# Kernel optimization log

Measured on AMD Instinct MI355X. Metric: run time of the kernel, lower is better.

## Reference

```python
import jax, jax.numpy as jnp
import numpy as np

MAX_SET_SIZE = 32  # f1_query_max_set_size


def setup_inputs() -> dict:
    key = jax.random.key(0)
    k1, k2, k3, k4 = jax.random.split(key, 4)
    B, Lq, L, d_qk, d_v = 8, 512, 4096, 64, 64
    q = jax.random.normal(k1, (B, Lq, d_qk), dtype=jnp.float32)
    k = jax.random.normal(k2, (B, L, d_qk), dtype=jnp.float32)
    v = jax.random.normal(k3, (B, L, d_v), dtype=jnp.float32)
    mask = jax.random.randint(k4, (B * Lq, L), 0, 2).astype(bool)
    return {"q": q, "k": k, "v": v, "mask": mask}


def _query_conditioned_subset_pool(rank_scores, v, batch_idx, mask, max_set_size):
    # rank_scores/mask: [N, L]; v: [B, L, d_v]
    N, L = rank_scores.shape
    keep = min(max_set_size, L)
    neg_inf = jnp.finfo(rank_scores.dtype).min
    masked_scores = jnp.where(mask, rank_scores.astype(jnp.float32), neg_inf)
    _, top_idx = jax.lax.top_k(masked_scores, keep)          # [N, keep]
    picked = jnp.take_along_axis(mask, top_idx, axis=1)
    sortable = jnp.where(picked, top_idx, L)                 # sentinel L for unpicked
    sortable = jnp.sort(sortable, axis=1)                    # restore index order
    picked = sortable < L
    safe_idx = jnp.where(picked, sortable, 0)                # [N, keep]
    sel_v = v[batch_idx[:, None], safe_idx]                  # [N, keep, d_v]
    sel_scores = jnp.take_along_axis(rank_scores, safe_idx, axis=1)
    sel_scores = jnp.where(picked, sel_scores, neg_inf)
    attn = jax.nn.softmax(sel_scores, axis=1)
    non_empty = picked.any(axis=1, keepdims=True)
    attn = jnp.where(picked & non_empty, attn, jnp.zeros_like(attn))
    return jnp.einsum('nk,nkd->nd', attn.astype(sel_v.dtype), sel_v)


def reference(q, k, v, mask):
    B, Lq, d_qk = q.shape
    L = k.shape[1]
    d_v = v.shape[-1]
    scale = 1.0 / float(np.sqrt(d_qk))
    # rank_scores [B, Lq, L] -> flat chains [B*Lq, L]
    rank_scores = jnp.einsum('bqd,bld->bql', q, k) * scale
    rs_flat = rank_scores.reshape(B * Lq, L)
    batch_idx = jnp.repeat(jnp.arange(B), Lq)
    # f1 = mean over masked support: sum_v / clamp(count, 1)
    mask_f = mask.astype(q.dtype)                            # [B*Lq, L]
    count = jnp.clip(mask_f.sum(axis=1), 1.0, None)          # [B*Lq]
    sum_v = jnp.einsum('bql,bld->bqd', mask_f.reshape(B, Lq, L), v).reshape(B * Lq, d_v)
    mean_out = sum_v / count[:, None]
    # f1_query_mode='add': query-conditioned restricted pooling over top-k subset
    q_ctx = _query_conditioned_subset_pool(rs_flat, v, batch_idx, mask, MAX_SET_SIZE)
    out = mean_out + q_ctx
    return out.reshape(B, Lq, d_v)
```

## Files before the change

### kernel.cpp

```cpp
#include <hip/hip_runtime.h>
#include <float.h>
#include <math.h>

#define LQ   512
#define LL   4096
#define DD   64
#define KEEP 32
#define NB   8
#define NROWS (NB * LQ)

#define WS_VT    (NROWS * LL)
#define WS_PC    (WS_VT + (NB * DD * LL) / 2)
#define WS_TOTAL (WS_PC + 4 * NROWS)

#define MASKED_KEY 0x00800000u

typedef short  bf16x8 __attribute__((ext_vector_type(8)));
typedef float  f32x4  __attribute__((ext_vector_type(4)));

__device__ __forceinline__ float dot4(float4 a, float4 b) {
    return a.x * b.x + a.y * b.y + a.z * b.z + a.w * b.w;
}
__device__ __forceinline__ unsigned short f2bf(float f) {
    unsigned int u = __float_as_uint(f);
    return (unsigned short)((u + 0x7FFFu + ((u >> 16) & 1u)) >> 16);
}

#define TP_LB 256
__global__ __launch_bounds__(256) void k_vt(
    const float* __restrict__ v, unsigned short* __restrict__ vt)
{
    __shared__ unsigned short tile[DD][TP_LB + 8];
    const int t  = threadIdx.x;
    const int b  = blockIdx.x >> 4;
    const int l0 = (blockIdx.x & 15) * TP_LB;

    const float4* vg = reinterpret_cast<const float4*>(v + ((size_t)b * LL + l0) * DD);
    #pragma unroll
    for (int i = 0; i < 16; ++i) {
        int j = t + 256 * i;
        float4 f = vg[j];
        int l = j >> 4, dq = (j & 15) * 4;
        tile[dq + 0][l] = f2bf(f.x);
        tile[dq + 1][l] = f2bf(f.y);
        tile[dq + 2][l] = f2bf(f.z);
        tile[dq + 3][l] = f2bf(f.w);
    }
    __syncthreads();
    const int d = t >> 2, seg = t & 3;
    const uint4* src = reinterpret_cast<const uint4*>(&tile[d][seg * 64]);
    uint4* dst = reinterpret_cast<uint4*>(vt + ((size_t)b * DD + d) * LL + l0 + seg * 64);
    #pragma unroll
    for (int i = 0; i < 8; ++i) dst[i] = src[i];
}

__global__ __launch_bounds__(256) void k_mean(
    const int* __restrict__ mask,
    const unsigned short* __restrict__ vt,
    float* __restrict__ out,
    float* __restrict__ pcnt)
{
    __shared__ float sums[4][4][16][16];
    __shared__ float cnt_s[4][16];

    const int t     = threadIdx.x;
    const int wave  = t >> 6;
    const int lane  = t & 63;
    const int lcq   = blockIdx.x & 3;
    const int rg    = blockIdx.x >> 2;
    const int n0    = rg * 16;
    const int b     = n0 / LQ;
    const int row_a = lane & 15;
    const int chunk = lane >> 4;
    const int lb    = lcq * 1024 + wave * 256;

    const int* mrow = mask + (size_t)(n0 + row_a) * LL + lb + chunk * 8;
    const unsigned short* vbase = vt + (size_t)b * DD * LL + lb + chunk * 8;

    f32x4 acc[4];
    #pragma unroll
    for (int dt = 0; dt < 4; ++dt) acc[dt] = (f32x4){0.f, 0.f, 0.f, 0.f};
    int cnt = 0;

    for (int l0 = 0; l0 < 256; l0 += 32) {
        int4 ma = *reinterpret_cast<const int4*>(mrow + l0);
        int4 mb = *reinterpret_cast<const int4*>(mrow + l0 + 4);
        cnt += (ma.x != 0) + (ma.y != 0) + (ma.z != 0) + (ma.w != 0)
             + (mb.x != 0) + (mb.y != 0) + (mb.z != 0) + (mb.w != 0);
        unsigned int p[4];
        p[0] = (ma.x ? 0x3F80u : 0u) | (ma.y ? 0x3F800000u : 0u);
        p[1] = (ma.z ? 0x3F80u : 0u) | (ma.w ? 0x3F800000u : 0u);
        p[2] = (mb.x ? 0x3F80u : 0u) | (mb.y ? 0x3F800000u : 0u);
        p[3] = (mb.z ? 0x3F80u : 0u) | (mb.w ? 0x3F800000u : 0u);
        bf16x8 afrag = *reinterpret_cast<bf16x8*>(p);
        #pragma unroll
        for (int dt = 0; dt < 4; ++dt) {
            bf16x8 bfrag = *reinterpret_cast<const bf16x8*>(
                vbase + (size_t)(dt * 16 + row_a) * LL + l0);
            acc[dt] = __builtin_amdgcn_mfma_f32_16x16x32_bf16(afrag, bfrag, acc[dt], 0, 0, 0);
        }
    }
    cnt += __shfl_xor(cnt, 16);
    cnt += __shfl_xor(cnt, 32);
    if (lane < 16) cnt_s[wave][lane] = (float)cnt;
    #pragma unroll
    for (int dt = 0; dt < 4; ++dt)
        #pragma unroll
        for (int r = 0; r < 4; ++r)
            sums[wave][dt][chunk * 4 + r][row_a] = acc[dt][r];
    __syncthreads();

    const int d = t & 63, rgrp = t >> 6;
    #pragma unroll
    for (int rr = 0; rr < 4; ++rr) {
        const int row = rgrp * 4 + rr;
        float s = sums[0][d >> 4][row][d & 15] + sums[1][d >> 4][row][d & 15]
                + sums[2][d >> 4][row][d & 15] + sums[3][d >> 4][row][d & 15];
        float c = cnt_s[0][row] + cnt_s[1][row] + cnt_s[2][row] + cnt_s[3][row];
        atomicAdd(&out[(size_t)(n0 + row) * DD + d], s);
        if (d == 0) pcnt[lcq * NROWS + n0 + row] = c;
    }
}

__global__ __launch_bounds__(256) void k_scores(
    const float* __restrict__ q,
    const float* __restrict__ kmat,
    const int*   __restrict__ mask,
    float*       __restrict__ ws_sc)
{
    const int t    = threadIdx.x;
    const int wave = t >> 6;
    const int lane = t & 63;
    const int lc   = blockIdx.x & 15;
    const int rg   = blockIdx.x >> 4;
    const int n0   = rg * 16;
    const int b    = n0 / LQ;
    const int l    = lc * 256 + wave * 64 + lane;

    const float4* kr = reinterpret_cast<const float4*>(kmat + ((size_t)b * LL + l) * DD);
    float4 kreg[16];
    #pragma unroll
    for (int i = 0; i < 16; ++i) kreg[i] = kr[i];

    int mreg[16];
    #pragma unroll
    for (int p = 0; p < 16; ++p)
        mreg[p] = mask[(size_t)(n0 + p) * LL + l];

    const int qb = __builtin_amdgcn_readfirstlane(n0 * DD);
    #pragma unroll
    for (int p = 0; p < 16; ++p) {
        const float4* qp = reinterpret_cast<const float4*>(q + qb + p * DD);
        float ax = 0.f, ay = 0.f, az = 0.f, aw = 0.f;
        #pragma unroll
        for (int i = 0; i < 16; ++i) {
            float4 qv = qp[i];
            ax = fmaf(qv.x, kreg[i].x, ax);
            ay = fmaf(qv.y, kreg[i].y, ay);
            az = fmaf(qv.z, kreg[i].z, az);
            aw = fmaf(qv.w, kreg[i].w, aw);
        }
        float acc = ax + ay + az + aw;
        ws_sc[(size_t)(n0 + p) * LL + l] = mreg[p] ? acc * 0.125f : -FLT_MAX;
    }
}

__global__ __launch_bounds__(256, 3) void k_select(
    const float* __restrict__ vmat,
    const float* __restrict__ ws,
    const float* __restrict__ pcnt,
    float*       __restrict__ out)
{
    __shared__ unsigned int hist[4][256];
    __shared__ unsigned int selKey[4][KEEP];
    __shared__ int          selIdx[4][KEEP];
    __shared__ float        wsel[4][KEEP];
    __shared__ int          selCnt[4], eqCnt[4];

    const int t    = threadIdx.x;
    const int wave = t >> 6;
    const int lane = t & 63;
    const int row  = blockIdx.x * 4 + wave;
    const int b    = row / LQ;

    float o = out[(size_t)row * DD + lane];
    {
        float cc = pcnt[row] + pcnt[NROWS + row]
                 + pcnt[2 * NROWS + row] + pcnt[3 * NROWS + row];
        if (cc < 1.f) cc = 1.f;
        o /= cc;
    }

    unsigned int key[64];
    {
        const float4* sg = reinterpret_cast<const float4*>(ws) + (size_t)row * (LL / 4);
        #pragma unroll
        for (int i = 0; i < 16; ++i) {
            float4 f = sg[lane + 64 * i];
            float vals[4] = { f.x, f.y, f.z, f.w };
            #pragma unroll
            for (int c = 0; c < 4; ++c) {
                unsigned int u = __float_as_uint(vals[c]);
                key[4 * i + c] = ((int)u < 0) ? ~u : (u | 0x80000000u);
            }
        }
    }

    unsigned int prefix = 0, quota = KEEP;
    #pragma unroll
    for (int pass = 0; pass < 4; ++pass) {
        const int shift = 24 - 8 * pass;
        const unsigned int hs = (pass == 0) ? 0u : (unsigned int)(32 - 8 * pass);
        reinterpret_cast<uint4*>(hist[wave])[lane] = make_uint4(0u, 0u, 0u, 0u);
        __asm__ volatile("s_waitcnt lgkmcnt(0)" ::: "memory");
        #pragma unroll
        for (int e = 0; e < 64; ++e) {
            bool act = (pass == 0) || ((key[e] >> hs) == prefix);
            if (act) atomicAdd(&hist[wave][(key[e] >> shift) & 255u], 1u);
        }
        __asm__ volatile("s_waitcnt lgkmcnt(0)" ::: "memory");
        uint4 h = reinterpret_cast<const uint4*>(hist[wave])[lane];
        unsigned int s4  = h.x + h.y + h.z + h.w;
        unsigned int suf = s4;
        #pragma unroll
        for (int off = 1; off < 64; off <<= 1) {
            unsigned int v = (unsigned int)__shfl_down((int)suf, off);
            if (lane + off < 64) suf += v;
        }
        unsigned int above = suf - s4;
        bool cond = (suf >= quota) && (above < quota);
        unsigned int Bq = 0, nq = 0;
        if (cond) {
            unsigned int hb[4] = { h.x, h.y, h.z, h.w };
            unsigned int run = above;
            int Bj = 0;
            #pragma unroll
            for (int j = 3; j >= 0; --j) {
                unsigned int nb = run + hb[j];
                if (nb >= quota) { Bj = j; break; }
                run = nb;
            }
            Bq = (unsigned int)(lane * 4 + Bj);
            nq = quota - run;
        }
        unsigned long long bal = __ballot(cond);
        int src = __ffsll(bal) - 1;
        Bq = (unsigned int)__shfl((int)Bq, src);
        nq = (unsigned int)__shfl((int)nq, src);
        prefix = (prefix << 8) | Bq;
        quota  = nq;
    }
    const unsigned int T = prefix;
    const bool take_eq = (T != MASKED_KEY);

    if (lane < KEEP) { wsel[wave][lane] = 0.f; selIdx[wave][lane] = 0; }
    if (lane == 0)   { selCnt[wave] = 0; eqCnt[wave] = 0; }
    __asm__ volatile("s_waitcnt lgkmcnt(0)" ::: "memory");
    #pragma unroll
    for (int e = 0; e < 64; ++e) {
        unsigned int k = key[e];
        if (k > T) {
            int slot = atomicAdd(&selCnt[wave], 1);
            selKey[wave][slot] = k;
            selIdx[wave][slot] = 256 * (e >> 2) + 4 * lane + (e & 3);
        } else if (take_eq && k == T) {
            int t2 = atomicAdd(&eqCnt[wave], 1);
            if (t2 < (int)quota) {
                int slot = atomicAdd(&selCnt[wave], 1);
                selKey[wave][slot] = k;
                selIdx[wave][slot] = 256 * (e >> 2) + 4 * lane + (e & 3);
            }
        }
    }
    __asm__ volatile("s_waitcnt lgkmcnt(0)" ::: "memory");
    const int S = selCnt[wave];

    if (S > 0) {
        float vj = -FLT_MAX;
        if (lane < S) {
            unsigned int kk = selKey[wave][lane];
            unsigned int u = (kk & 0x80000000u) ? (kk ^ 0x80000000u) : ~kk;
            vj = __uint_as_float(u);
        }
        float mx = vj;
        #pragma unroll
        for (int off = 1; off < 64; off <<= 1) mx = fmaxf(mx, __shfl_xor(mx, off));
        float e = (lane < S) ? expf(vj - mx) : 0.f;
        float sum = e;
        #pragma unroll
        for (int off = 1; off < 64; off <<= 1) sum += __shfl_xor(sum, off);
        if (lane < S) wsel[wave][lane] = e / sum;
        __asm__ volatile("s_waitcnt lgkmcnt(0)" ::: "memory");
        const float* vb = vmat + (size_t)b * LL * DD + lane;
        #pragma unroll
        for (int j = 0; j < KEEP; ++j) {
            float wj = wsel[wave][j];
            int   ij = selIdx[wave][j];
            o += wj * vb[(size_t)ij * DD];
        }
    }
    out[(size_t)row * DD + lane] = o;
}

#define QT   2
#define NT   256
#define NTILES (LL / NT)

__global__ __launch_bounds__(NT, 4) void ga_fused_fb(
    const float* __restrict__ q, const float* __restrict__ kmat,
    const float* __restrict__ vmat, const int* __restrict__ mask,
    float* __restrict__ out)
{
    __shared__ float sc[QT][LL];
    __shared__ float q_s[QT][DD];
    __shared__ unsigned long long mbits[QT][LL / 64];
    __shared__ float redv[4][QT][DD];
    __shared__ float mean_s[QT][DD];
    __shared__ int   count_s[QT];
    __shared__ int   sel_idx[QT][KEEP];
    __shared__ float sel_val[QT][KEEP];
    __shared__ int   sel_cnt[QT];
    __shared__ float wred[4];
    __shared__ int   ired[4];
    __shared__ int   brk;
    __shared__ float wgt[QT][KEEP];

    const int t = threadIdx.x, wave = t >> 6, lane = t & 63;
    const int n0 = blockIdx.x * QT, b = n0 / LQ;

    if (t < QT) sel_cnt[t] = 0;
    if (t < QT * DD) q_s[t >> 6][t & 63] = q[(size_t)(n0 + (t >> 6)) * DD + (t & 63)];
    __syncthreads();

    const float4* q4_0 = reinterpret_cast<const float4*>(&q_s[0][0]);
    const float4* q4_1 = reinterpret_cast<const float4*>(&q_s[1][0]);
    for (int tile = 0; tile < NTILES; ++tile) {
        int l = tile * NT + t;
        const float4* kr = reinterpret_cast<const float4*>(kmat + (size_t)(b * LL + l) * DD);
        float d0 = 0.f, d1 = 0.f;
        #pragma unroll
        for (int i = 0; i < 16; ++i) {
            float4 kk = kr[i], qa = q4_0[i], qb = q4_1[i];
            d0 += kk.x * qa.x + kk.y * qa.y + kk.z * qa.z + kk.w * qa.w;
            d1 += kk.x * qb.x + kk.y * qb.y + kk.z * qb.z + kk.w * qb.w;
        }
        int mv0 = mask[(size_t)n0 * LL + l];
        int mv1 = mask[(size_t)(n0 + 1) * LL + l];
        unsigned long long b0 = __ballot(mv0 != 0);
        unsigned long long b1 = __ballot(mv1 != 0);
        if (lane == 0) { mbits[0][tile * 4 + wave] = b0; mbits[1][tile * 4 + wave] = b1; }
        sc[0][l] = mv0 ? d0 * 0.125f : -FLT_MAX;
        sc[1][l] = mv1 ? d1 * 0.125f : -FLT_MAX;
    }
    __syncthreads();

    if (wave < QT) {
        int c = (int)__popcll(mbits[wave][lane]);
        for (int off = 32; off >= 1; off >>= 1) c += __shfl_down(c, off);
        if (lane == 0) count_s[wave] = c;
    }
    {
        float acc0 = 0.f, acc1 = 0.f;
        const int g = wave, d = lane;
        for (int wi = 0; wi < LL / 64; ++wi) {
            unsigned long long w0 = mbits[0][wi], w1 = mbits[1][wi];
            const float* vp = vmat + (size_t)(b * LL + wi * 64 + g) * DD + d;
            #pragma unroll 4
            for (int ii = 0; ii < 16; ++ii) {
                int sh = g + 4 * ii;
                float vv = vp[(size_t)(4 * ii) * DD];
                if ((w0 >> sh) & 1ULL) acc0 += vv;
                if ((w1 >> sh) & 1ULL) acc1 += vv;
            }
        }
        redv[g][0][d] = acc0; redv[g][1][d] = acc1;
    }
    __syncthreads();
    if (t < QT * DD) {
        int qt = t >> 6, dd = t & 63;
        float s2 = redv[0][qt][dd] + redv[1][qt][dd] + redv[2][qt][dd] + redv[3][qt][dd];
        int c = count_s[qt]; if (c < 1) c = 1;
        mean_s[qt][dd] = s2 / (float)c;
    }
    __syncthreads();

    for (int qt = 0; qt < QT; ++qt) {
        for (int s = 0; s < KEEP; ++s) {
            float m = -FLT_MAX; int mi = LL;
            for (int j = 0; j < NTILES; ++j) {
                int l = j * NT + t;
                float val = sc[qt][l];
                if (val > m) { m = val; mi = l; }
            }
            for (int off = 32; off >= 1; off >>= 1) {
                float ov = __shfl_down(m, off);
                int   oi = __shfl_down(mi, off);
                if (ov > m || (ov == m && oi < mi)) { m = ov; mi = oi; }
            }
            if (lane == 0) { wred[wave] = m; ired[wave] = mi; }
            __syncthreads();
            if (t == 0) {
                float bv = wred[0]; int bi = ired[0];
                for (int w2 = 1; w2 < 4; ++w2) {
                    float ov = wred[w2]; int oi = ired[w2];
                    if (ov > bv || (ov == bv && oi < bi)) { bv = ov; bi = oi; }
                }
                if (bv > -FLT_MAX) {
                    sel_idx[qt][s] = bi; sel_val[qt][s] = bv; sel_cnt[qt] = s + 1;
                    sc[qt][bi] = -FLT_MAX; brk = 0;
                } else brk = 1;
            }
            __syncthreads();
            if (brk) break;
        }
    }

    if (wave < QT) {
        int qt = wave, S = sel_cnt[qt];
        if (S > 0) {
            float mx = sel_val[qt][0];
            float e = 0.f;
            if (lane < S) e = expf(sel_val[qt][lane] - mx);
            float ssum = e;
            for (int off = 32; off >= 1; off >>= 1) ssum += __shfl_xor(ssum, off);
            if (lane < S) wgt[qt][lane] = e / ssum;
        }
    }
    __syncthreads();
    if (wave < QT) {
        int qt = wave, S = sel_cnt[qt];
        float o = mean_s[qt][lane];
        for (int j = 0; j < S; ++j)
            o += wgt[qt][j] * vmat[(size_t)(b * LL + sel_idx[qt][j]) * DD + lane];
        out[(size_t)(n0 + qt) * DD + lane] = o;
    }
}

extern "C" void kernel_launch(void* const* d_in, const int* in_sizes, int n_in,
                              void* d_out, int out_size, void* d_ws, size_t ws_size,
                              hipStream_t stream) {
    const float* q    = (const float*)d_in[0];
    const float* kmat = (const float*)d_in[1];
    const float* vmat = (const float*)d_in[2];
    const int*   mask = (const int*)d_in[3];
    float* out = (float*)d_out;

    const size_t need = (size_t)WS_TOTAL * sizeof(float);
    if (ws_size >= need) {
        float* ws = (float*)d_ws;
        unsigned short* vt = (unsigned short*)(ws + WS_VT);
        float* pcnt = ws + WS_PC;
        hipMemsetAsync(out, 0, (size_t)NROWS * DD * sizeof(float), stream);
        hipLaunchKernelGGL(k_scores, dim3(4096), dim3(256), 0, stream,
                           q, kmat, mask, ws);
        hipLaunchKernelGGL(k_vt, dim3(NB * 16), dim3(256), 0, stream, vmat, vt);
        hipLaunchKernelGGL(k_mean, dim3((NROWS / 16) * 4), dim3(256), 0, stream,
                           mask, vt, out, pcnt);
        hipLaunchKernelGGL(k_select, dim3(NROWS / 4), dim3(256), 0, stream,
                           vmat, ws, pcnt, out);
    } else {
        hipLaunchKernelGGL(ga_fused_fb, dim3(NROWS / QT), dim3(NT), 0, stream,
                           q, kmat, vmat, mask, out);
    }
}
```

Measured before the change: 253.7 us.

## Fuse masked mean accumulation into score kernel using ballot-packed mask bits

Removes the separate k_mean kernel and computes the masked V sum and count inside k_scores. The mask values it already loads are packed with ballots into shared bitmasks and fed as bf16 MFMA operands against the transposed V. The intent is to avoid reading the 64 MB int mask a second time. The costs are more global atomics (16x more blocks each add partial sums into out and a single pcnt), an extra memset, and higher register and LDS pressure in k_scores.

```diff
diff --git a/kernel.cpp b/kernel.cpp
--- a/kernel.cpp
+++ b/kernel.cpp
@@ -54,80 +54,19 @@
     for (int i = 0; i < 8; ++i) dst[i] = src[i];
 }
 
-__global__ __launch_bounds__(256) void k_mean(
-    const int* __restrict__ mask,
-    const unsigned short* __restrict__ vt,
-    float* __restrict__ out,
-    float* __restrict__ pcnt)
-{
-    __shared__ float sums[4][4][16][16];
-    __shared__ float cnt_s[4][16];
-
-    const int t     = threadIdx.x;
-    const int wave  = t >> 6;
-    const int lane  = t & 63;
-    const int lcq   = blockIdx.x & 3;
-    const int rg    = blockIdx.x >> 2;
-    const int n0    = rg * 16;
-    const int b     = n0 / LQ;
-    const int row_a = lane & 15;
-    const int chunk = lane >> 4;
-    const int lb    = lcq * 1024 + wave * 256;
-
-    const int* mrow = mask + (size_t)(n0 + row_a) * LL + lb + chunk * 8;
-    const unsigned short* vbase = vt + (size_t)b * DD * LL + lb + chunk * 8;
-
-    f32x4 acc[4];
-    #pragma unroll
-    for (int dt = 0; dt < 4; ++dt) acc[dt] = (f32x4){0.f, 0.f, 0.f, 0.f};
-    int cnt = 0;
-
-    for (int l0 = 0; l0 < 256; l0 += 32) {
-        int4 ma = *reinterpret_cast<const int4*>(mrow + l0);
-        int4 mb = *reinterpret_cast<const int4*>(mrow + l0 + 4);
-        cnt += (ma.x != 0) + (ma.y != 0) + (ma.z != 0) + (ma.w != 0)
-             + (mb.x != 0) + (mb.y != 0) + (mb.z != 0) + (mb.w != 0);
-        unsigned int p[4];
-        p[0] = (ma.x ? 0x3F80u : 0u) | (ma.y ? 0x3F800000u : 0u);
-        p[1] = (ma.z ? 0x3F80u : 0u) | (ma.w ? 0x3F800000u : 0u);
-        p[2] = (mb.x ? 0x3F80u : 0u) | (mb.y ? 0x3F800000u : 0u);
-        p[3] = (mb.z ? 0x3F80u : 0u) | (mb.w ? 0x3F800000u : 0u);
-        bf16x8 afrag = *reinterpret_cast<bf16x8*>(p);
-        #pragma unroll
-        for (int dt = 0; dt < 4; ++dt) {
-            bf16x8 bfrag = *reinterpret_cast<const bf16x8*>(
-                vbase + (size_t)(dt * 16 + row_a) * LL + l0);
-            acc[dt] = __builtin_amdgcn_mfma_f32_16x16x32_bf16(afrag, bfrag, acc[dt], 0, 0, 0);
-        }
-    }
-    cnt += __shfl_xor(cnt, 16);
-    cnt += __shfl_xor(cnt, 32);
-    if (lane < 16) cnt_s[wave][lane] = (float)cnt;
-    #pragma unroll
-    for (int dt = 0; dt < 4; ++dt)
-        #pragma unroll
-        for (int r = 0; r < 4; ++r)
-            sums[wave][dt][chunk * 4 + r][row_a] = acc[dt][r];
-    __syncthreads();
-
-    const int d = t & 63, rgrp = t >> 6;
-    #pragma unroll
-    for (int rr = 0; rr < 4; ++rr) {
-        const int row = rgrp * 4 + rr;
-        float s = sums[0][d >> 4][row][d & 15] + sums[1][d >> 4][row][d & 15]
-                + sums[2][d >> 4][row][d & 15] + sums[3][d >> 4][row][d & 15];
-        float c = cnt_s[0][row] + cnt_s[1][row] + cnt_s[2][row] + cnt_s[3][row];
-        atomicAdd(&out[(size_t)(n0 + row) * DD + d], s);
-        if (d == 0) pcnt[lcq * NROWS + n0 + row] = c;
-    }
-}
-
 __global__ __launch_bounds__(256) void k_scores(
     const float* __restrict__ q,
     const float* __restrict__ kmat,
     const int*   __restrict__ mask,
-    float*       __restrict__ ws_sc)
+    const unsigned short* __restrict__ vt,
+    float*       __restrict__ ws_sc,
+    float*       __restrict__ out,
+    float*       __restrict__ pcnt)
 {
+    __shared__ unsigned long long bits64[4][16];
+    __shared__ float sums[4][4][16][16];
+    __shared__ float cnt_s[4][16];
+
     const int t    = threadIdx.x;
     const int wave = t >> 6;
     const int lane = t & 63;
@@ -137,15 +76,77 @@
     const int b    = n0 / LQ;
     const int l    = lc * 256 + wave * 64 + lane;
 
+    int mreg[16];
+    #pragma unroll
+    for (int p = 0; p < 16; ++p)
+        mreg[p] = mask[(size_t)(n0 + p) * LL + l];
+
+    unsigned long long bl[16];
+    #pragma unroll
+    for (int p = 0; p < 16; ++p) bl[p] = __ballot(mreg[p] != 0);
+    if (lane == 0) {
+        #pragma unroll
+        for (int p = 0; p < 16; ++p) bits64[wave][p] = bl[p];
+    }
+    __asm__ volatile("s_waitcnt lgkmcnt(0)" ::: "memory");
+
+    {
+        const int row_a = lane & 15;
+        const int chunk = lane >> 4;
+        const unsigned char* bb =
+            reinterpret_cast<const unsigned char*>(&bits64[wave][row_a]);
+        const unsigned short* vtb =
+            vt + (size_t)b * DD * LL + lc * 256 + wave * 64 + chunk * 8;
+
+        f32x4 acc[4];
+        #pragma unroll
+        for (int dt = 0; dt < 4; ++dt) acc[dt] = (f32x4){0.f, 0.f, 0.f, 0.f};
+
+        #pragma unroll
+        for (int s = 0; s < 2; ++s) {
+            const unsigned int byte = bb[s * 4 + chunk];
+            unsigned int pk[4];
+            pk[0] = ((byte & 1u)   ? 0x3F80u : 0u) | ((byte & 2u)   ? 0x3F800000u : 0u);
+            pk[1] = ((byte & 4u)   ? 0x3F80u : 0u) | ((byte & 8u)   ? 0x3F800000u : 0u);
+            pk[2] = ((byte & 16u)  ? 0x3F80u : 0u) | ((byte & 32u)  ? 0x3F800000u : 0u);
+            pk[3] = ((byte & 64u)  ? 0x3F80u : 0u) | ((byte & 128u) ? 0x3F800000u : 0u);
+            bf16x8 afrag = *reinterpret_cast<bf16x8*>(pk);
+            #pragma unroll
+            for (int dt = 0; dt < 4; ++dt) {
+                bf16x8 bfrag = *reinterpret_cast<const bf16x8*>(
+                    vtb + (size_t)(dt * 16 + row_a) * LL + s * 32);
+                acc[dt] = __builtin_amdgcn_mfma_f32_16x16x32_bf16(afrag, bfrag, acc[dt], 0, 0, 0);
+            }
+        }
+        #pragma unroll
+        for (int dt = 0; dt < 4; ++dt)
+            #pragma unroll
+            for (int r = 0; r < 4; ++r)
+                sums[wave][dt][chunk * 4 + r][row_a] = acc[dt][r];
+        if (lane < 16)
+            cnt_s[wave][lane] = (float)__popcll(bits64[wave][lane]);
+    }
+    __syncthreads();
+
+    {
+        const int d = t & 63, rgrp = t >> 6;
+        #pragma unroll
+        for (int rr = 0; rr < 4; ++rr) {
+            const int row = rgrp * 4 + rr;
+            float s = sums[0][d >> 4][row][d & 15] + sums[1][d >> 4][row][d & 15]
+                    + sums[2][d >> 4][row][d & 15] + sums[3][d >> 4][row][d & 15];
+            atomicAdd(&out[(size_t)(n0 + row) * DD + d], s);
+        }
+        if (t < 16) {
+            float c = cnt_s[0][t] + cnt_s[1][t] + cnt_s[2][t] + cnt_s[3][t];
+            atomicAdd(&pcnt[n0 + t], c);
+        }
+    }
+
     const float4* kr = reinterpret_cast<const float4*>(kmat + ((size_t)b * LL + l) * DD);
     float4 kreg[16];
     #pragma unroll
     for (int i = 0; i < 16; ++i) kreg[i] = kr[i];
-
-    int mreg[16];
-    #pragma unroll
-    for (int p = 0; p < 16; ++p)
-        mreg[p] = mask[(size_t)(n0 + p) * LL + l];
 
     const int qb = __builtin_amdgcn_readfirstlane(n0 * DD);
     #pragma unroll
@@ -185,8 +186,7 @@
 
     float o = out[(size_t)row * DD + lane];
     {
-        float cc = pcnt[row] + pcnt[NROWS + row]
-                 + pcnt[2 * NROWS + row] + pcnt[3 * NROWS + row];
+        float cc = pcnt[row];
         if (cc < 1.f) cc = 1.f;
         o /= cc;
     }
@@ -451,11 +451,10 @@
         unsigned short* vt = (unsigned short*)(ws + WS_VT);
         float* pcnt = ws + WS_PC;
         hipMemsetAsync(out, 0, (size_t)NROWS * DD * sizeof(float), stream);
+        hipMemsetAsync(pcnt, 0, (size_t)NROWS * sizeof(float), stream);
+        hipLaunchKernelGGL(k_vt, dim3(NB * 16), dim3(256), 0, stream, vmat, vt);
         hipLaunchKernelGGL(k_scores, dim3(4096), dim3(256), 0, stream,
-                           q, kmat, mask, ws);
-        hipLaunchKernelGGL(k_vt, dim3(NB * 16), dim3(256), 0, stream, vmat, vt);
-        hipLaunchKernelGGL(k_mean, dim3((NROWS / 16) * 4), dim3(256), 0, stream,
-                           mask, vt, out, pcnt);
+                           q, kmat, mask, vt, ws, out, pcnt);
         hipLaunchKernelGGL(k_select, dim3(NROWS / 4), dim3(256), 0, stream,
                            vmat, ws, pcnt, out);
     } else {
```

New measurement: 253.6 us. About the same (-0.0%).
